# Kernel tuning notes

Measured on AMD Instinct MI355X. Metric: run time of the kernel, lower is better.

The kernel has to match this reference:

```python
import jax, jax.numpy as jnp
import numpy as np

N, E, D_IN, D_H, D_OUT = 50000, 600000, 128, 128, 1


def setup_inputs() -> dict:
    key = jax.random.key(0)
    ks = jax.random.split(key, 20)
    p = lambda k, sh: jax.random.normal(k, sh, dtype=jnp.float32) * 0.05
    return {
        "x": jax.random.normal(ks[0], (N, D_IN), dtype=jnp.float32),
        "edge_weight": jax.random.uniform(ks[1], (E,), dtype=jnp.float32),
        # input LEConv (lin1: W1/b1, lin2: W2 no bias, lin3: W3/b3)
        "W1_in": p(ks[2], (D_IN, D_H)), "b1_in": jnp.zeros((D_H,), jnp.float32),
        "W2_in": p(ks[3], (D_IN, D_H)),
        "W3_in": p(ks[4], (D_IN, D_H)), "b3_in": jnp.zeros((D_H,), jnp.float32),
        # inner LEConv
        "W1_h": p(ks[5], (D_H, D_H)), "b1_h": jnp.zeros((D_H,), jnp.float32),
        "W2_h": p(ks[6], (D_H, D_H)),
        "W3_h": p(ks[7], (D_H, D_H)), "b3_h": jnp.zeros((D_H,), jnp.float32),
        # output LEConv
        "W1_o": p(ks[8], (D_H, D_OUT)), "b1_o": jnp.zeros((D_OUT,), jnp.float32),
        "W2_o": p(ks[9], (D_H, D_OUT)),
        "W3_o": p(ks[10], (D_H, D_OUT)), "b3_o": jnp.zeros((D_OUT,), jnp.float32),
        # LayerNorms
        "g1": jnp.ones((D_H,), jnp.float32), "beta1": jnp.zeros((D_H,), jnp.float32),
        "g2": jnp.ones((D_H,), jnp.float32), "beta2": jnp.zeros((D_H,), jnp.float32),
        "edge_index": jax.random.randint(ks[11], (2, E), 0, N, dtype=jnp.int32),
        "number_of_layers": 4,
    }


def _leconv(x, src, dst, w, W1, b1, W2, W3, b3):
    # PyG LEConv: out_i = lin3(x_i) + sum_{j->i} w_e * (lin1(x_j) - lin2(x_i))
    a = x @ W1 + b1                                   # [N, D_out]
    b = x @ W2                                        # [N, D_out]
    wsum = jax.ops.segment_sum(w, dst, num_segments=N)             # [N]
    agg = jax.ops.segment_sum(w[:, None] * a[src], dst, num_segments=N)  # [N, D_out]
    return agg - b * wsum[:, None] + x @ W3 + b3


def _ln(x, g, b, eps=1e-5):
    m = x.mean(-1, keepdims=True)
    v = x.var(-1, keepdims=True)
    return (x - m) * jax.lax.rsqrt(v + eps) * g + b


def reference(x, edge_weight, W1_in, b1_in, W2_in, W3_in, b3_in,
              W1_h, b1_h, W2_h, W3_h, b3_h,
              W1_o, b1_o, W2_o, W3_o, b3_o,
              g1, beta1, g2, beta2, edge_index, number_of_layers):
    src, dst = edge_index[0], edge_index[1]
    # per-feature standardization over nodes (torch std is unbiased -> ddof=1)
    x = (x - x.mean(0, keepdims=True)) / (jnp.std(x, axis=0, ddof=1, keepdims=True) + 1e-6)
    h = jax.nn.leaky_relu(
        _ln(_leconv(x, src, dst, edge_weight, W1_in, b1_in, W2_in, W3_in, b3_in), g1, beta1),
        negative_slope=0.1)
    for _ in range(number_of_layers - 2):
        h = jax.nn.leaky_relu(
            _ln(_leconv(h, src, dst, edge_weight, W1_h, b1_h, W2_h, W3_h, b3_h), g2, beta2),
            negative_slope=0.1)
    h = _leconv(h, src, dst, edge_weight, W1_o, b1_o, W2_o, W3_o, b3_o)
    return jax.nn.sigmoid(h)
```

## Files before the change

### kernel.cpp

```cpp
#include <hip/hip_runtime.h>
#include <hip/hip_bf16.h>
#include <math.h>


typedef _Float16 f16x8 __attribute__((ext_vector_type(8)));
typedef _Float16 f16x4 __attribute__((ext_vector_type(4)));
typedef float f32x4 __attribute__((ext_vector_type(4)));

#define LSTRIDE 136
#define CS_BLOCKS 512
#define WFIX 8388608.0f
#define DPAD 16


__global__ __launch_bounds__(256) void prep_kernel(
    const float* __restrict__ x, int N,
    float* __restrict__ ps, float* __restrict__ pss,
    const float* __restrict__ W1a, const float* __restrict__ W2a,
    const float* __restrict__ W3a, _Float16* __restrict__ Wta,
    const float* __restrict__ W1b, const float* __restrict__ W2b,
    const float* __restrict__ W3b, _Float16* __restrict__ Wtb,
    unsigned long long* __restrict__ degw, int* __restrict__ counter)
{
    __shared__ float shs[256][4];
    __shared__ float shq[256][4];
    int bid = blockIdx.x;
    int t = threadIdx.x;

    if (bid < CS_BLOCKS) {
        int g = t >> 5;
        int c = t & 31;
        const float4* xv = (const float4*)x;
        const int S = CS_BLOCKS * 8;
        float s0=0.f,s1=0.f,s2=0.f,s3=0.f, q0=0.f,q1=0.f,q2=0.f,q3=0.f;
        int r = bid * 8 + g;
        for (; r + 3*S < N; r += 4*S) {
            float4 v0 = xv[(size_t)r * 32 + c];
            float4 v1 = xv[(size_t)(r + S) * 32 + c];
            float4 v2 = xv[(size_t)(r + 2*S) * 32 + c];
            float4 v3 = xv[(size_t)(r + 3*S) * 32 + c];
            s0 += v0.x + v1.x + v2.x + v3.x;
            s1 += v0.y + v1.y + v2.y + v3.y;
            s2 += v0.z + v1.z + v2.z + v3.z;
            s3 += v0.w + v1.w + v2.w + v3.w;
            q0 += v0.x*v0.x + v1.x*v1.x + v2.x*v2.x + v3.x*v3.x;
            q1 += v0.y*v0.y + v1.y*v1.y + v2.y*v2.y + v3.y*v3.y;
            q2 += v0.z*v0.z + v1.z*v1.z + v2.z*v2.z + v3.z*v3.z;
            q3 += v0.w*v0.w + v1.w*v1.w + v2.w*v2.w + v3.w*v3.w;
        }
        for (; r < N; r += S) {
            float4 v = xv[(size_t)r * 32 + c];
            s0 += v.x; s1 += v.y; s2 += v.z; s3 += v.w;
            q0 += v.x*v.x; q1 += v.y*v.y; q2 += v.z*v.z; q3 += v.w*v.w;
        }
        shs[t][0]=s0; shs[t][1]=s1; shs[t][2]=s2; shs[t][3]=s3;
        shq[t][0]=q0; shq[t][1]=q1; shq[t][2]=q2; shq[t][3]=q3;
        __syncthreads();
        if (t < 32) {
            float S4[4] = {0,0,0,0}, Q4[4] = {0,0,0,0};
            #pragma unroll
            for (int gg = 0; gg < 8; ++gg) {
                #pragma unroll
                for (int i = 0; i < 4; ++i) {
                    S4[i] += shs[t + 32*gg][i];
                    Q4[i] += shq[t + 32*gg][i];
                }
            }
            #pragma unroll
            for (int i = 0; i < 4; ++i) {
                ps [bid * 128 + t*4 + i] = S4[i];
                pss[bid * 128 + t*4 + i] = Q4[i];
            }
        }
        return;
    }

    if (bid < CS_BLOCKS + 384) {
        int idx = (bid - CS_BLOCKS) * 256 + t;
        int set = idx >= 384 * 128;
        int id = idx - set * 384 * 128;
        int n = id >> 7, k = id & 127;
        const float* W = set ? ((n < 128) ? W1b : (n < 256) ? W2b : W3b)
                             : ((n < 128) ? W1a : (n < 256) ? W2a : W3a);
        _Float16* Wt = set ? Wtb : Wta;
        int c = n & 127;
        Wt[id] = (_Float16)W[k * 128 + c];
        return;
    }

    int idx = (bid - CS_BLOCKS - 384) * 256 + t;
    int tot = N * DPAD;
    for (int i = idx; i < tot; i += 128 * 256) degw[i] = 0ULL;
    if (idx == 0) { counter[0] = 0; counter[64] = 0; }
}


__global__ __launch_bounds__(256) void hist_pack_kernel(
    const int* __restrict__ dst, const float* __restrict__ ew,
    unsigned long long* __restrict__ degw, int* __restrict__ rank, int E)
{
    int e = blockIdx.x * 256 + threadIdx.x;
    if (e < E) {
        int d = dst[e];
        unsigned int wf = __float2uint_rn(ew[e] * WFIX);
        unsigned long long old =
            atomicAdd(&degw[(size_t)d * DPAD], (1ULL << 32) | (unsigned long long)wf);
        rank[e] = (int)(old >> 32);
    }
}

__global__ __launch_bounds__(256) void scan_fused_kernel(
    const unsigned long long* __restrict__ degw, int N,
    float* __restrict__ wsum, int* __restrict__ rowptr, int E,
    int* __restrict__ partial, int* __restrict__ counter)
{
    __shared__ int sh[256];
    __shared__ int lastFlag;
    __shared__ int blockOff;
    int t = threadIdx.x;
    int base = blockIdx.x * 1024 + t * 4;
    int v[4]; int s = 0;
    #pragma unroll
    for (int i = 0; i < 4; ++i) {
        int idx = base + i;
        if (idx < N) {
            unsigned long long w = degw[(size_t)idx * DPAD];
            v[i] = (int)(w >> 32);
            wsum[idx] = (float)(unsigned int)w * (1.0f / WFIX);
        } else v[i] = 0;
        s += v[i];
    }
    sh[t] = s; __syncthreads();
    for (int off = 1; off < 256; off <<= 1) {
        int x = sh[t];
        if (t >= off) x += sh[t - off];
        __syncthreads();
        sh[t] = x;
        __syncthreads();
    }
    if (t == 0) {
        atomicExch(&partial[blockIdx.x], sh[255]);
        __threadfence();
        int tk = atomicAdd(&counter[0], 1);
        lastFlag = (tk == (int)gridDim.x - 1) ? 1 : 0;
    }
    __syncthreads();
    if (lastFlag) {
        if (t < 64) {
            __threadfence();
            int nb = (int)gridDim.x;
            int o = (t < nb) ? atomicAdd(&partial[t], 0) : 0;
            int vv = o;
            #pragma unroll
            for (int off = 1; off < 64; off <<= 1) {
                int u = __shfl_up(vv, off, 64);
                if (t >= off) vv += u;
            }
            if (t < nb) atomicExch(&partial[t], vv - o);
        }
        __syncthreads();
        if (t == 0) { __threadfence(); atomicExch(&counter[64], 1); }
    }
    if (t == 0) {
        while (atomicAdd(&counter[64], 0) == 0) {}
        __threadfence();
        blockOff = atomicAdd(&partial[blockIdx.x], 0);
    }
    __syncthreads();
    int off0 = blockOff + ((t > 0) ? sh[t - 1] : 0);
    #pragma unroll
    for (int i = 0; i < 4; ++i) {
        int idx = base + i;
        if (idx < N) { rowptr[idx] = off0; off0 += v[i]; }
    }
    if (blockIdx.x == 0 && t == 0) rowptr[N] = E;
}

__global__ __launch_bounds__(256) void csr_fill_stats_kernel(
    const int* __restrict__ src, const int* __restrict__ dst,
    const float* __restrict__ ew, const int* __restrict__ rowptr,
    const int* __restrict__ rank, int2* __restrict__ csr, int E, int eBlocks,
    const float* __restrict__ ps, const float* __restrict__ pss, int Nn,
    float* __restrict__ mean, float* __restrict__ rstd)
{
    int bid = blockIdx.x;
    int t = threadIdx.x;
    if (bid < eBlocks) {
        int e = bid * 256 + t;
        if (e >= E) return;
        int d = dst[e];
        int pos = rowptr[d] + rank[e];
        csr[pos] = make_int2(src[e], __float_as_int(ew[e]));
        return;
    }
    __shared__ float sh1[256], sh2[256];
    int f = bid - eBlocks;
    int r0 = t * 2;
    float s1 = ps [(size_t)r0 * 128 + f] + ps [(size_t)(r0 + 1) * 128 + f];
    float s2 = pss[(size_t)r0 * 128 + f] + pss[(size_t)(r0 + 1) * 128 + f];
    sh1[t] = s1; sh2[t] = s2; __syncthreads();
    for (int off = 128; off > 0; off >>= 1) {
        if (t < off) { sh1[t] += sh1[t + off]; sh2[t] += sh2[t + off]; }
        __syncthreads();
    }
    if (t == 0) {
        float sum = sh1[0], sumsq = sh2[0];
        float m = sum / (float)Nn;
        float var = (sumsq - sum * sum / (float)Nn) / (float)(Nn - 1);
        var = fmaxf(var, 0.f);
        mean[f] = m;
        rstd[f] = 1.f / (sqrtf(var) + 1e-6f);
    }
}


__global__ __launch_bounds__(256, 2) void gemm_mfma_kernel(
    const _Float16* __restrict__ h, int N, int nTiles,
    const _Float16* __restrict__ Wt,
    const float* __restrict__ b1,
    const float* __restrict__ b3,
    const float* __restrict__ wsum,
    _Float16* __restrict__ out_a, _Float16* __restrict__ out_d)
{
    __shared__ _Float16 ldsS[64 * LSTRIDE];
    __shared__ _Float16 lds_a[64 * LSTRIDE];
    __shared__ _Float16 lds_d[64 * LSTRIDE];

    int t = threadIdx.x;
    int wave = t >> 6;
    int lane = t & 63;
    int quad = lane >> 4;
    int c16  = lane & 15;

    const f16x8* wv = (const f16x8*)Wt;
    int ntl[6] = {2*wave, 2*wave+1, 8+2*wave, 9+2*wave, 16+2*wave, 17+2*wave};
    f16x8 bfrag[6][4];
    #pragma unroll
    for (int j = 0; j < 6; ++j) {
        int nrow = ntl[j] * 16 + c16;
        #pragma unroll
        for (int s = 0; s < 4; ++s)
            bfrag[j][s] = wv[(size_t)nrow * 16 + s * 4 + quad];
    }
    float bb1[2], bb3[2];
    #pragma unroll
    for (int j = 0; j < 2; ++j) {
        int col = (2*wave + j) * 16 + c16;
        bb1[j] = b1[col];
        bb3[j] = b3[col];
    }

    const f16x8* hv = (const f16x8*)h;
    f16x8* oa = (f16x8*)out_a;
    f16x8* od = (f16x8*)out_d;

    for (int tile = blockIdx.x; tile < nTiles; tile += gridDim.x) {
        int row0 = tile * 64;

        #pragma unroll
        for (int i = 0; i < 4; ++i) {
            int idx = i * 256 + t;
            int row = idx >> 4;
            int chunk = idx & 15;
            int grow = row0 + row;
            if (grow >= N) grow = N - 1;
            *(f16x8*)&ldsS[row * LSTRIDE + chunk * 8] = hv[(size_t)grow * 16 + chunk];
        }
        __syncthreads();

        #pragma unroll
        for (int r = 0; r < 4; ++r) {
            f16x8 afrag[4];
            #pragma unroll
            for (int s = 0; s < 4; ++s)
                afrag[s] = *(const f16x8*)&ldsS[(r*16 + c16) * LSTRIDE + (s*4 + quad) * 8];

            f32x4 acc[6];
            #pragma unroll
            for (int j = 0; j < 6; ++j) acc[j] = (f32x4){0.f, 0.f, 0.f, 0.f};
            #pragma unroll
            for (int s = 0; s < 4; ++s) {
                #pragma unroll
                for (int j = 0; j < 6; ++j)
                    acc[j] = __builtin_amdgcn_mfma_f32_16x16x32_f16(afrag[s], bfrag[j][s], acc[j], 0, 0, 0);
            }

            float wsv[4];
            #pragma unroll
            for (int reg = 0; reg < 4; ++reg) {
                int gr = row0 + r*16 + quad*4 + reg;
                wsv[reg] = wsum[(gr < N) ? gr : (N - 1)];
            }
            #pragma unroll
            for (int j = 0; j < 2; ++j) {
                int col = (2*wave + j) * 16 + c16;
                #pragma unroll
                for (int reg = 0; reg < 4; ++reg) {
                    int lr = r*16 + quad*4 + reg;
                    lds_a[lr * LSTRIDE + col] = (_Float16)(acc[j][reg] + bb1[j]);
                    lds_d[lr * LSTRIDE + col] =
                        (_Float16)(acc[4+j][reg] + bb3[j] - wsv[reg] * acc[2+j][reg]);
                }
            }
        }
        __syncthreads();

        #pragma unroll
        for (int i = 0; i < 4; ++i) {
            int idx = i * 256 + t;
            int row = idx >> 4;
            int c8  = idx & 15;
            int grow = row0 + row;
            if (grow < N) {
                f16x8 va = *(const f16x8*)&lds_a[row * LSTRIDE + c8 * 8];
                oa[(size_t)grow * 16 + c8] = va;
                f16x8 vd = *(const f16x8*)&lds_d[row * LSTRIDE + c8 * 8];
                od[(size_t)grow * 16 + c8] = vd;
            }
        }
        __syncthreads();
    }
}


__global__ __launch_bounds__(256, 2) void gemm_mfma_std_kernel(
    const float* __restrict__ x,
    const float* __restrict__ meanp, const float* __restrict__ rstdp,
    int N, int nTiles,
    const _Float16* __restrict__ Wt,
    const float* __restrict__ b1,
    const float* __restrict__ b3,
    const float* __restrict__ wsum,
    _Float16* __restrict__ out_a, _Float16* __restrict__ out_d)
{
    __shared__ _Float16 ldsS[64 * LSTRIDE];
    __shared__ _Float16 lds_a[64 * LSTRIDE];
    __shared__ _Float16 lds_d[64 * LSTRIDE];

    int t = threadIdx.x;
    int wave = t >> 6;
    int lane = t & 63;
    int quad = lane >> 4;
    int c16  = lane & 15;

    const f16x8* wv = (const f16x8*)Wt;
    int ntl[6] = {2*wave, 2*wave+1, 8+2*wave, 9+2*wave, 16+2*wave, 17+2*wave};
    f16x8 bfrag[6][4];
    #pragma unroll
    for (int j = 0; j < 6; ++j) {
        int nrow = ntl[j] * 16 + c16;
        #pragma unroll
        for (int s = 0; s < 4; ++s)
            bfrag[j][s] = wv[(size_t)nrow * 16 + s * 4 + quad];
    }
    float bb1[2], bb3[2];
    #pragma unroll
    for (int j = 0; j < 2; ++j) {
        int col = (2*wave + j) * 16 + c16;
        bb1[j] = b1[col];
        bb3[j] = b3[col];
    }

    int c4 = t & 31;
    float4 mu = ((const float4*)meanp)[c4];
    float4 rs = ((const float4*)rstdp)[c4];

    const float4* xv = (const float4*)x;
    f16x8* oa = (f16x8*)out_a;
    f16x8* od = (f16x8*)out_d;

    for (int tile = blockIdx.x; tile < nTiles; tile += gridDim.x) {
        int row0 = tile * 64;

        #pragma unroll
        for (int i = 0; i < 8; ++i) {
            int idx = i * 256 + t;
            int row = idx >> 5;
            int grow = row0 + row;
            if (grow >= N) grow = N - 1;
            float4 v = xv[(size_t)grow * 32 + c4];
            f16x4 o;
            o.x = (_Float16)((v.x - mu.x) * rs.x);
            o.y = (_Float16)((v.y - mu.y) * rs.y);
            o.z = (_Float16)((v.z - mu.z) * rs.z);
            o.w = (_Float16)((v.w - mu.w) * rs.w);
            *(f16x4*)&ldsS[row * LSTRIDE + c4 * 4] = o;
        }
        __syncthreads();

        #pragma unroll
        for (int r = 0; r < 4; ++r) {
            f16x8 afrag[4];
            #pragma unroll
            for (int s = 0; s < 4; ++s)
                afrag[s] = *(const f16x8*)&ldsS[(r*16 + c16) * LSTRIDE + (s*4 + quad) * 8];

            f32x4 acc[6];
            #pragma unroll
            for (int j = 0; j < 6; ++j) acc[j] = (f32x4){0.f, 0.f, 0.f, 0.f};
            #pragma unroll
            for (int s = 0; s < 4; ++s) {
                #pragma unroll
                for (int j = 0; j < 6; ++j)
                    acc[j] = __builtin_amdgcn_mfma_f32_16x16x32_f16(afrag[s], bfrag[j][s], acc[j], 0, 0, 0);
            }

            float wsv[4];
            #pragma unroll
            for (int reg = 0; reg < 4; ++reg) {
                int gr = row0 + r*16 + quad*4 + reg;
                wsv[reg] = wsum[(gr < N) ? gr : (N - 1)];
            }
            #pragma unroll
            for (int j = 0; j < 2; ++j) {
                int col = (2*wave + j) * 16 + c16;
                #pragma unroll
                for (int reg = 0; reg < 4; ++reg) {
                    int lr = r*16 + quad*4 + reg;
                    lds_a[lr * LSTRIDE + col] = (_Float16)(acc[j][reg] + bb1[j]);
                    lds_d[lr * LSTRIDE + col] =
                        (_Float16)(acc[4+j][reg] + bb3[j] - wsv[reg] * acc[2+j][reg]);
                }
            }
        }
        __syncthreads();

        #pragma unroll
        for (int i = 0; i < 4; ++i) {
            int idx = i * 256 + t;
            int row = idx >> 4;
            int c8  = idx & 15;
            int grow = row0 + row;
            if (grow < N) {
                f16x8 va = *(const f16x8*)&lds_a[row * LSTRIDE + c8 * 8];
                oa[(size_t)grow * 16 + c8] = va;
                f16x8 vd = *(const f16x8*)&lds_d[row * LSTRIDE + c8 * 8];
                od[(size_t)grow * 16 + c8] = vd;
            }
        }
        __syncthreads();
    }
}


__global__ __launch_bounds__(256) void aggregate_ln_kernel(
    const int* __restrict__ rowptr, const int2* __restrict__ csr,
    const _Float16* __restrict__ a, const _Float16* __restrict__ d,
    const float* __restrict__ g, const float* __restrict__ beta,
    _Float16* __restrict__ out, int N)
{
    int wave = threadIdx.x >> 6;
    int lane = threadIdx.x & 63;
    int grp  = lane >> 4;
    int l    = lane & 15;
    int node = blockIdx.x * 4 + wave;
    if (node >= N) return;
    int b = rowptr[node], en = rowptr[node + 1];
    int deg = en - b;

    const f16x8* av = (const f16x8*)a;
    f16x8 dv = ((const f16x8*)d)[(size_t)node * 16 + l];
    float acc[8] = {0,0,0,0,0,0,0,0};

    int nk = (deg + 3) >> 2;
    int k = 0;
    for (; k + 4 <= nk; k += 4) {
        int2 p[4];
        #pragma unroll
        for (int j = 0; j < 4; ++j) {
            int idx = b + (k + j) * 4 + grp;
            int idc = (idx < en) ? idx : b;
            p[j] = csr[idc];
            if (idx >= en) p[j].y = 0;
        }
        f16x8 v[4];
        #pragma unroll
        for (int j = 0; j < 4; ++j)
            v[j] = av[(size_t)p[j].x * 16 + l];
        #pragma unroll
        for (int j = 0; j < 4; ++j) {
            float w = __int_as_float(p[j].y);
            #pragma unroll
            for (int i = 0; i < 8; ++i) acc[i] += w * (float)v[j][i];
        }
    }
    if (k < nk) {
        int2 p[4];
        #pragma unroll
        for (int j = 0; j < 4; ++j) {
            int idx = b + (k + j) * 4 + grp;
            int idc = (idx < en) ? idx : b;
            p[j] = csr[idc];
            if (idx >= en) p[j].y = 0;
        }
        f16x8 v[4];
        #pragma unroll
        for (int j = 0; j < 4; ++j)
            v[j] = av[(size_t)p[j].x * 16 + l];
        #pragma unroll
        for (int j = 0; j < 4; ++j) {
            float w = __int_as_float(p[j].y);
            #pragma unroll
            for (int i = 0; i < 8; ++i) acc[i] += w * (float)v[j][i];
        }
    }

    #pragma unroll
    for (int i = 0; i < 8; ++i) {
        acc[i] += __shfl_xor(acc[i], 16, 64);
        acc[i] += __shfl_xor(acc[i], 32, 64);
    }

    float v[8];
    float s = 0.f, ss = 0.f;
    #pragma unroll
    for (int i = 0; i < 8; ++i) {
        v[i] = acc[i] + (float)dv[i];
        s += v[i]; ss += v[i] * v[i];
    }
    #pragma unroll
    for (int off = 1; off <= 8; off <<= 1) {
        s  += __shfl_xor(s,  off, 64);
        ss += __shfl_xor(ss, off, 64);
    }
    float mean = s * (1.f / 128.f);
    float var = ss * (1.f / 128.f) - mean * mean;
    float rstd = rsqrtf(var + 1e-5f);

    const float4* gv4 = (const float4*)g;
    const float4* bv4 = (const float4*)beta;
    float4 ga = gv4[l*2], gb = gv4[l*2+1];
    float4 ba = bv4[l*2], bb = bv4[l*2+1];
    float go[8] = {ga.x,ga.y,ga.z,ga.w,gb.x,gb.y,gb.z,gb.w};
    float bo[8] = {ba.x,ba.y,ba.z,ba.w,bb.x,bb.y,bb.z,bb.w};
    f16x8 ov;
    #pragma unroll
    for (int i = 0; i < 8; ++i) {
        float o = (v[i] - mean) * rstd * go[i] + bo[i];
        o = o >= 0.f ? o : 0.1f * o;
        ov[i] = (_Float16)o;
    }
    if (grp == 0)
        ((f16x8*)out)[(size_t)node * 16 + l] = ov;
}


__global__ __launch_bounds__(256) void aggregate_out_kernel(
    const int* __restrict__ rowptr, const int2* __restrict__ csr,
    const _Float16* __restrict__ a, const _Float16* __restrict__ d,
    const float* __restrict__ g, const float* __restrict__ beta,
    const float* __restrict__ W1o, const float* __restrict__ b1o,
    const float* __restrict__ W2o,
    const float* __restrict__ W3o, const float* __restrict__ b3o,
    const float* __restrict__ wsum,
    float* __restrict__ a1, float* __restrict__ dpart, int N)
{
    int wave = threadIdx.x >> 6;
    int lane = threadIdx.x & 63;
    int grp  = lane >> 4;
    int l    = lane & 15;
    int node = blockIdx.x * 4 + wave;
    if (node >= N) return;
    int b = rowptr[node], en = rowptr[node + 1];
    int deg = en - b;

    const f16x8* av = (const f16x8*)a;
    f16x8 dv = ((const f16x8*)d)[(size_t)node * 16 + l];
    float wsn = wsum[node];
    float acc[8] = {0,0,0,0,0,0,0,0};

    int nk = (deg + 3) >> 2;
    int k = 0;
    for (; k + 4 <= nk; k += 4) {
        int2 p[4];
        #pragma unroll
        for (int j = 0; j < 4; ++j) {
            int idx = b + (k + j) * 4 + grp;
            int idc = (idx < en) ? idx : b;
            p[j] = csr[idc];
            if (idx >= en) p[j].y = 0;
        }
        f16x8 v[4];
        #pragma unroll
        for (int j = 0; j < 4; ++j)
            v[j] = av[(size_t)p[j].x * 16 + l];
        #pragma unroll
        for (int j = 0; j < 4; ++j) {
            float w = __int_as_float(p[j].y);
            #pragma unroll
            for (int i = 0; i < 8; ++i) acc[i] += w * (float)v[j][i];
        }
    }
    if (k < nk) {
        int2 p[4];
        #pragma unroll
        for (int j = 0; j < 4; ++j) {
            int idx = b + (k + j) * 4 + grp;
            int idc = (idx < en) ? idx : b;
            p[j] = csr[idc];
            if (idx >= en) p[j].y = 0;
        }
        f16x8 v[4];
        #pragma unroll
        for (int j = 0; j < 4; ++j)
            v[j] = av[(size_t)p[j].x * 16 + l];
        #pragma unroll
        for (int j = 0; j < 4; ++j) {
            float w = __int_as_float(p[j].y);
            #pragma unroll
            for (int i = 0; i < 8; ++i) acc[i] += w * (float)v[j][i];
        }
    }

    #pragma unroll
    for (int i = 0; i < 8; ++i) {
        acc[i] += __shfl_xor(acc[i], 16, 64);
        acc[i] += __shfl_xor(acc[i], 32, 64);
    }

    float v[8];
    float s = 0.f, ss = 0.f;
    #pragma unroll
    for (int i = 0; i < 8; ++i) {
        v[i] = acc[i] + (float)dv[i];
        s += v[i]; ss += v[i] * v[i];
    }
    #pragma unroll
    for (int off = 1; off <= 8; off <<= 1) {
        s  += __shfl_xor(s,  off, 64);
        ss += __shfl_xor(ss, off, 64);
    }
    float mean = s * (1.f / 128.f);
    float var = ss * (1.f / 128.f) - mean * mean;
    float rstd = rsqrtf(var + 1e-5f);

    const float4* gv4 = (const float4*)g;
    const float4* bv4 = (const float4*)beta;
    float4 ga = gv4[l*2], gb = gv4[l*2+1];
    float4 ba = bv4[l*2], bb = bv4[l*2+1];
    float go[8] = {ga.x,ga.y,ga.z,ga.w,gb.x,gb.y,gb.z,gb.w};
    float bo[8] = {ba.x,ba.y,ba.z,ba.w,bb.x,bb.y,bb.z,bb.w};

    float ho[8];
    #pragma unroll
    for (int i = 0; i < 8; ++i) {
        float o = (v[i] - mean) * rstd * go[i] + bo[i];
        o = o >= 0.f ? o : 0.1f * o;
        ho[i] = (float)(_Float16)o;
    }

    const float4* w1v = (const float4*)W1o;
    const float4* w2v = (const float4*)W2o;
    const float4* w3v = (const float4*)W3o;
    float4 w1a = w1v[l*2], w1b = w1v[l*2+1];
    float4 w2a = w2v[l*2], w2b = w2v[l*2+1];
    float4 w3a = w3v[l*2], w3b = w3v[l*2+1];
    float s1 = ho[0]*w1a.x + ho[1]*w1a.y + ho[2]*w1a.z + ho[3]*w1a.w
             + ho[4]*w1b.x + ho[5]*w1b.y + ho[6]*w1b.z + ho[7]*w1b.w;
    float s2 = ho[0]*w2a.x + ho[1]*w2a.y + ho[2]*w2a.z + ho[3]*w2a.w
             + ho[4]*w2b.x + ho[5]*w2b.y + ho[6]*w2b.z + ho[7]*w2b.w;
    float s3 = ho[0]*w3a.x + ho[1]*w3a.y + ho[2]*w3a.z + ho[3]*w3a.w
             + ho[4]*w3b.x + ho[5]*w3b.y + ho[6]*w3b.z + ho[7]*w3b.w;
    #pragma unroll
    for (int off = 1; off <= 8; off <<= 1) {
        s1 += __shfl_xor(s1, off, 64);
        s2 += __shfl_xor(s2, off, 64);
        s3 += __shfl_xor(s3, off, 64);
    }
    if (lane == 0) {
        a1[node] = s1 + b1o[0];
        dpart[node] = s3 + b3o[0] - wsn * s2;
    }
}


__global__ __launch_bounds__(256) void gather_out_kernel(
    const int* __restrict__ rowptr, const int2* __restrict__ csr,
    const float* __restrict__ a1, const float* __restrict__ dpart,
    float* __restrict__ out, int N)
{
    int n = blockIdx.x * 256 + threadIdx.x;
    if (n >= N) return;
    int b = rowptr[n], en = rowptr[n + 1];
    float s = dpart[n];
    int e = b;
    for (; e + 4 <= en; e += 4) {
        int2 p0 = csr[e], p1 = csr[e+1], p2 = csr[e+2], p3 = csr[e+3];
        float x0 = a1[p0.x], x1 = a1[p1.x], x2 = a1[p2.x], x3 = a1[p3.x];
        s += __int_as_float(p0.y) * x0 + __int_as_float(p1.y) * x1
           + __int_as_float(p2.y) * x2 + __int_as_float(p3.y) * x3;
    }
    for (; e < en; ++e) {
        int2 p = csr[e];
        s += __int_as_float(p.y) * a1[p.x];
    }
    out[n] = 1.f / (1.f + expf(-s));
}

extern "C" void kernel_launch(void* const* d_in, const int* in_sizes, int n_in,
                              void* d_out, int out_size, void* d_ws, size_t ws_size,
                              hipStream_t stream)
{
    const float* x     = (const float*)d_in[0];
    const float* ew    = (const float*)d_in[1];
    const float* W1_in = (const float*)d_in[2];
    const float* b1_in = (const float*)d_in[3];
    const float* W2_in = (const float*)d_in[4];
    const float* W3_in = (const float*)d_in[5];
    const float* b3_in = (const float*)d_in[6];
    const float* W1_h  = (const float*)d_in[7];
    const float* b1_h  = (const float*)d_in[8];
    const float* W2_h  = (const float*)d_in[9];
    const float* W3_h  = (const float*)d_in[10];
    const float* b3_h  = (const float*)d_in[11];
    const float* W1_o  = (const float*)d_in[12];
    const float* b1_o  = (const float*)d_in[13];
    const float* W2_o  = (const float*)d_in[14];
    const float* W3_o  = (const float*)d_in[15];
    const float* b3_o  = (const float*)d_in[16];
    const float* g1    = (const float*)d_in[17];
    const float* beta1 = (const float*)d_in[18];
    const float* g2    = (const float*)d_in[19];
    const float* beta2 = (const float*)d_in[20];
    const int*   eidx  = (const int*)d_in[21];

    const int N = in_sizes[0] / 128;
    const int E = in_sizes[1];
    const int* srcp = eidx;
    const int* dstp = eidx + E;

    size_t off = 0;
    auto carve = [&](size_t nbytes) -> void* {
        void* p = (char*)d_ws + off;
        off += (nbytes + 255) & ~(size_t)255;
        return p;
    };
    unsigned long long* degw = (unsigned long long*)carve((size_t)N * DPAD * 8);
    int*      rank   = (int*)     carve((size_t)E * 4);
    _Float16* buf_h  = (_Float16*)carve((size_t)N * 128 * 2);
    _Float16* buf_a  = (_Float16*)carve((size_t)N * 128 * 2);
    _Float16* buf_d  = (_Float16*)carve((size_t)N * 128 * 2);
    int2*     csr    = (int2*)    carve((size_t)E * 8);
    _Float16* Wt_in  = (_Float16*)carve(384 * 128 * 2);
    _Float16* Wt_h   = (_Float16*)carve(384 * 128 * 2);
    int*      rowptr = (int*)     carve((size_t)(N + 1) * 4);
    int*      partial= (int*)     carve(256 * 4);
    int*      counter= (int*)     carve(256 * 4);
    float*    ps     = (float*)   carve((size_t)CS_BLOCKS * 128 * 4);
    float*    pss    = (float*)   carve((size_t)CS_BLOCKS * 128 * 4);
    float*    meanp  = (float*)   carve(128 * 4);
    float*    rstdp  = (float*)   carve(128 * 4);
    float*    wsum   = (float*)   carve((size_t)N * 4);
    float*    a1     = (float*)   carve((size_t)N * 4);
    float*    dpart  = (float*)   carve((size_t)N * 4);

    const int nodeWaveBlocks = (N + 3) / 4;
    const int eBlocks = (E + 255) / 256;
    const int nBlocks = (N + 255) / 256;
    const int nb = (N + 1023) / 1024;

    prep_kernel<<<CS_BLOCKS + 384 + 128, 256, 0, stream>>>(
        x, N, ps, pss,
        W1_in, W2_in, W3_in, Wt_in, W1_h, W2_h, W3_h, Wt_h,
        degw, counter);

    hist_pack_kernel<<<eBlocks, 256, 0, stream>>>(dstp, ew, degw, rank, E);

    scan_fused_kernel<<<nb, 256, 0, stream>>>(degw, N, wsum, rowptr, E, partial, counter);

    csr_fill_stats_kernel<<<eBlocks + 128, 256, 0, stream>>>(
        srcp, dstp, ew, rowptr, rank, csr, E, eBlocks,
        ps, pss, N, meanp, rstdp);

    const int nTiles = (N + 63) / 64;
    const int gemmGrid = (nTiles < 512) ? nTiles : 512;

    gemm_mfma_std_kernel<<<gemmGrid, 256, 0, stream>>>(
        x, meanp, rstdp, N, nTiles, Wt_in, b1_in, b3_in, wsum, buf_a, buf_d);
    aggregate_ln_kernel<<<nodeWaveBlocks, 256, 0, stream>>>(rowptr, csr, buf_a, buf_d, g1, beta1, buf_h, N);

    gemm_mfma_kernel<<<gemmGrid, 256, 0, stream>>>(buf_h, N, nTiles, Wt_h, b1_h, b3_h, wsum, buf_a, buf_d);
    aggregate_ln_kernel<<<nodeWaveBlocks, 256, 0, stream>>>(rowptr, csr, buf_a, buf_d, g2, beta2, buf_h, N);

    gemm_mfma_kernel<<<gemmGrid, 256, 0, stream>>>(buf_h, N, nTiles, Wt_h, b1_h, b3_h, wsum, buf_a, buf_d);
    aggregate_out_kernel<<<nodeWaveBlocks, 256, 0, stream>>>(
        rowptr, csr, buf_a, buf_d, g2, beta2,
        W1_o, b1_o, W2_o, W3_o, b3_o, wsum, a1, dpart, N);

    gather_out_kernel<<<nBlocks, 256, 0, stream>>>(rowptr, csr, a1, dpart, (float*)d_out, N);
}
```

Before: 307.1 us.

## Move column-stats reduction into histogram kernel and widen GEMM grid

The per-feature sum and sum-of-squares reduction over x moves out of prep_kernel into the edge histogram kernel as extra blocks. The memory-bound stats read can then overlap with the atomic-bound degree histogram, and prep becomes a small kernel. The GEMM kernels drop the min-2-blocks launch bound and the persistent grid cap grows from 512 to 768. That gives the compiler more register freedom, but occupancy may fall if register use rises.

```diff
diff --git a/kernel.cpp b/kernel.cpp
--- a/kernel.cpp
+++ b/kernel.cpp
@@ -14,69 +14,18 @@
 
 
 __global__ __launch_bounds__(256) void prep_kernel(
-    const float* __restrict__ x, int N,
-    float* __restrict__ ps, float* __restrict__ pss,
+    int N,
     const float* __restrict__ W1a, const float* __restrict__ W2a,
     const float* __restrict__ W3a, _Float16* __restrict__ Wta,
     const float* __restrict__ W1b, const float* __restrict__ W2b,
     const float* __restrict__ W3b, _Float16* __restrict__ Wtb,
     unsigned long long* __restrict__ degw, int* __restrict__ counter)
 {
-    __shared__ float shs[256][4];
-    __shared__ float shq[256][4];
     int bid = blockIdx.x;
     int t = threadIdx.x;
 
-    if (bid < CS_BLOCKS) {
-        int g = t >> 5;
-        int c = t & 31;
-        const float4* xv = (const float4*)x;
-        const int S = CS_BLOCKS * 8;
-        float s0=0.f,s1=0.f,s2=0.f,s3=0.f, q0=0.f,q1=0.f,q2=0.f,q3=0.f;
-        int r = bid * 8 + g;
-        for (; r + 3*S < N; r += 4*S) {
-            float4 v0 = xv[(size_t)r * 32 + c];
-            float4 v1 = xv[(size_t)(r + S) * 32 + c];
-            float4 v2 = xv[(size_t)(r + 2*S) * 32 + c];
-            float4 v3 = xv[(size_t)(r + 3*S) * 32 + c];
-            s0 += v0.x + v1.x + v2.x + v3.x;
-            s1 += v0.y + v1.y + v2.y + v3.y;
-            s2 += v0.z + v1.z + v2.z + v3.z;
-            s3 += v0.w + v1.w + v2.w + v3.w;
-            q0 += v0.x*v0.x + v1.x*v1.x + v2.x*v2.x + v3.x*v3.x;
-            q1 += v0.y*v0.y + v1.y*v1.y + v2.y*v2.y + v3.y*v3.y;
-            q2 += v0.z*v0.z + v1.z*v1.z + v2.z*v2.z + v3.z*v3.z;
-            q3 += v0.w*v0.w + v1.w*v1.w + v2.w*v2.w + v3.w*v3.w;
-        }
-        for (; r < N; r += S) {
-            float4 v = xv[(size_t)r * 32 + c];
-            s0 += v.x; s1 += v.y; s2 += v.z; s3 += v.w;
-            q0 += v.x*v.x; q1 += v.y*v.y; q2 += v.z*v.z; q3 += v.w*v.w;
-        }
-        shs[t][0]=s0; shs[t][1]=s1; shs[t][2]=s2; shs[t][3]=s3;
-        shq[t][0]=q0; shq[t][1]=q1; shq[t][2]=q2; shq[t][3]=q3;
-        __syncthreads();
-        if (t < 32) {
-            float S4[4] = {0,0,0,0}, Q4[4] = {0,0,0,0};
-            #pragma unroll
-            for (int gg = 0; gg < 8; ++gg) {
-                #pragma unroll
-                for (int i = 0; i < 4; ++i) {
-                    S4[i] += shs[t + 32*gg][i];
-                    Q4[i] += shq[t + 32*gg][i];
-                }
-            }
-            #pragma unroll
-            for (int i = 0; i < 4; ++i) {
-                ps [bid * 128 + t*4 + i] = S4[i];
-                pss[bid * 128 + t*4 + i] = Q4[i];
-            }
-        }
-        return;
-    }
-
-    if (bid < CS_BLOCKS + 384) {
-        int idx = (bid - CS_BLOCKS) * 256 + t;
+    if (bid < 384) {
+        int idx = bid * 256 + t;
         int set = idx >= 384 * 128;
         int id = idx - set * 384 * 128;
         int n = id >> 7, k = id & 127;
@@ -88,24 +37,81 @@
         return;
     }
 
-    int idx = (bid - CS_BLOCKS - 384) * 256 + t;
+    int idx = (bid - 384) * 256 + t;
     int tot = N * DPAD;
     for (int i = idx; i < tot; i += 128 * 256) degw[i] = 0ULL;
     if (idx == 0) { counter[0] = 0; counter[64] = 0; }
 }
 
 
-__global__ __launch_bounds__(256) void hist_pack_kernel(
+__global__ __launch_bounds__(256) void hist_cs_kernel(
     const int* __restrict__ dst, const float* __restrict__ ew,
-    unsigned long long* __restrict__ degw, int* __restrict__ rank, int E)
-{
-    int e = blockIdx.x * 256 + threadIdx.x;
-    if (e < E) {
-        int d = dst[e];
-        unsigned int wf = __float2uint_rn(ew[e] * WFIX);
-        unsigned long long old =
-            atomicAdd(&degw[(size_t)d * DPAD], (1ULL << 32) | (unsigned long long)wf);
-        rank[e] = (int)(old >> 32);
+    unsigned long long* __restrict__ degw, int* __restrict__ rank, int E,
+    int eBlocks,
+    const float* __restrict__ x, int N,
+    float* __restrict__ ps, float* __restrict__ pss)
+{
+    int bid = blockIdx.x;
+    int t = threadIdx.x;
+
+    if (bid < eBlocks) {
+        int e = bid * 256 + t;
+        if (e < E) {
+            int d = dst[e];
+            unsigned int wf = __float2uint_rn(ew[e] * WFIX);
+            unsigned long long old =
+                atomicAdd(&degw[(size_t)d * DPAD], (1ULL << 32) | (unsigned long long)wf);
+            rank[e] = (int)(old >> 32);
+        }
+        return;
+    }
+
+    __shared__ float shs[256][4];
+    __shared__ float shq[256][4];
+    int cb = bid - eBlocks;
+    int g = t >> 5;
+    int c = t & 31;
+    const float4* xv = (const float4*)x;
+    const int S = CS_BLOCKS * 8;
+    float s0=0.f,s1=0.f,s2=0.f,s3=0.f, q0=0.f,q1=0.f,q2=0.f,q3=0.f;
+    int r = cb * 8 + g;
+    for (; r + 3*S < N; r += 4*S) {
+        float4 v0 = xv[(size_t)r * 32 + c];
+        float4 v1 = xv[(size_t)(r + S) * 32 + c];
+        float4 v2 = xv[(size_t)(r + 2*S) * 32 + c];
+        float4 v3 = xv[(size_t)(r + 3*S) * 32 + c];
+        s0 += v0.x + v1.x + v2.x + v3.x;
+        s1 += v0.y + v1.y + v2.y + v3.y;
+        s2 += v0.z + v1.z + v2.z + v3.z;
+        s3 += v0.w + v1.w + v2.w + v3.w;
+        q0 += v0.x*v0.x + v1.x*v1.x + v2.x*v2.x + v3.x*v3.x;
+        q1 += v0.y*v0.y + v1.y*v1.y + v2.y*v2.y + v3.y*v3.y;
+        q2 += v0.z*v0.z + v1.z*v1.z + v2.z*v2.z + v3.z*v3.z;
+        q3 += v0.w*v0.w + v1.w*v1.w + v2.w*v2.w + v3.w*v3.w;
+    }
+    for (; r < N; r += S) {
+        float4 v = xv[(size_t)r * 32 + c];
+        s0 += v.x; s1 += v.y; s2 += v.z; s3 += v.w;
+        q0 += v.x*v.x; q1 += v.y*v.y; q2 += v.z*v.z; q3 += v.w*v.w;
+    }
+    shs[t][0]=s0; shs[t][1]=s1; shs[t][2]=s2; shs[t][3]=s3;
+    shq[t][0]=q0; shq[t][1]=q1; shq[t][2]=q2; shq[t][3]=q3;
+    __syncthreads();
+    if (t < 32) {
+        float S4[4] = {0,0,0,0}, Q4[4] = {0,0,0,0};
+        #pragma unroll
+        for (int gg = 0; gg < 8; ++gg) {
+            #pragma unroll
+            for (int i = 0; i < 4; ++i) {
+                S4[i] += shs[t + 32*gg][i];
+                Q4[i] += shq[t + 32*gg][i];
+            }
+        }
+        #pragma unroll
+        for (int i = 0; i < 4; ++i) {
+            ps [cb * 128 + t*4 + i] = S4[i];
+            pss[cb * 128 + t*4 + i] = Q4[i];
+        }
     }
 }
 
@@ -214,7 +220,7 @@
 }
 
 
-__global__ __launch_bounds__(256, 2) void gemm_mfma_kernel(
+__global__ __launch_bounds__(256) void gemm_mfma_kernel(
     const _Float16* __restrict__ h, int N, int nTiles,
     const _Float16* __restrict__ Wt,
     const float* __restrict__ b1,
@@ -323,7 +329,7 @@
 }
 
 
-__global__ __launch_bounds__(256, 2) void gemm_mfma_std_kernel(
+__global__ __launch_bounds__(256) void gemm_mfma_std_kernel(
     const float* __restrict__ x,
     const float* __restrict__ meanp, const float* __restrict__ rstdp,
     int N, int nTiles,
@@ -759,12 +765,12 @@
     const int nBlocks = (N + 255) / 256;
     const int nb = (N + 1023) / 1024;
 
-    prep_kernel<<<CS_BLOCKS + 384 + 128, 256, 0, stream>>>(
-        x, N, ps, pss,
-        W1_in, W2_in, W3_in, Wt_in, W1_h, W2_h, W3_h, Wt_h,
+    prep_kernel<<<512, 256, 0, stream>>>(
+        N, W1_in, W2_in, W3_in, Wt_in, W1_h, W2_h, W3_h, Wt_h,
         degw, counter);
 
-    hist_pack_kernel<<<eBlocks, 256, 0, stream>>>(dstp, ew, degw, rank, E);
+    hist_cs_kernel<<<eBlocks + CS_BLOCKS, 256, 0, stream>>>(
+        dstp, ew, degw, rank, E, eBlocks, x, N, ps, pss);
 
     scan_fused_kernel<<<nb, 256, 0, stream>>>(degw, N, wsum, rowptr, E, partial, counter);
 
@@ -773,7 +779,7 @@
         ps, pss, N, meanp, rstdp);
 
     const int nTiles = (N + 63) / 64;
-    const int gemmGrid = (nTiles < 512) ? nTiles : 512;
+    const int gemmGrid = (nTiles < 768) ? nTiles : 768;
 
     gemm_mfma_std_kernel<<<gemmGrid, 256, 0, stream>>>(
         x, meanp, rstdp, N, nTiles, Wt_in, b1_in, b3_in, wsum, buf_a, buf_d);
```

After: 314.5 us. 1.02x slower.
